# Kernel optimization log

Hardware: AMD Instinct MI355X
Metric: run time of the kernel (lower is better)

Reference implementation:

```python
import jax, jax.numpy as jnp
import numpy as np

N_NODES = 50000
N_EDGES = 800000
N_REL = 16
D = 64          # entity_dim == relation_dim == n_hidden
NEG_SLOPE = 0.01  # torch F.leaky_relu default


def setup_inputs() -> dict:
    key = jax.random.key(0)
    ks = jax.random.split(key, 12)
    s = 1.0 / np.sqrt(D)
    return {
        "node_ids": jnp.arange(N_NODES, dtype=jnp.int64) if jax.config.jax_enable_x64 else jnp.arange(N_NODES, dtype=jnp.int32),
        "relation_ids": jax.random.randint(ks[0], (N_EDGES,), 0, N_REL),
        "src": jax.random.randint(ks[1], (N_EDGES,), 0, N_NODES),
        "dst": jax.random.randint(ks[2], (N_EDGES,), 0, N_NODES),
        "entity_embed": jax.random.normal(ks[3], (N_NODES, D), jnp.float32) * s,
        "relation_embed": jax.random.normal(ks[4], (N_REL, D), jnp.float32) * s,
        "W0": jax.random.normal(ks[5], (N_REL, D, D), jnp.float32) * s,
        "W1": jax.random.normal(ks[6], (N_REL, D, D), jnp.float32) * s,
        "ra0": jax.random.normal(ks[7], (D, D), jnp.float32) * s,
        "rb0": jax.random.normal(ks[8], (D, D), jnp.float32) * s,
        "ra1": jax.random.normal(ks[9], (D, D), jnp.float32) * s,
        "rb1": jax.random.normal(ks[10], (D, D), jnp.float32) * s,
    }


def _edge_softmax(scores, dst, n_nodes):
    # segment softmax over edges grouped by destination node (DGL edge_softmax)
    m = jax.ops.segment_max(scores, dst, num_segments=n_nodes)  # [N]
    e = jnp.exp(scores - m[dst])                                # [E]
    z = jax.ops.segment_sum(e, dst, num_segments=n_nodes)       # [N]
    return e / z[dst]


def _kgat_layer(h, efeat, src, dst, etype, Wr, ra, rb, n_nodes):
    # transform every node under every relation once: [N, R, Dr]
    trans = jnp.einsum('nd,rde->nre', h, Wr)
    t_r = trans[src, etype]                   # W_r h_t  [E, Dr]
    h_r = trans[dst, etype]                   # W_r h_h  [E, Dr]
    att = jnp.sum(t_r * jnp.tanh(h_r + efeat), axis=1)  # [E]
    a = _edge_softmax(att, dst, n_nodes)                 # [E]
    # u_mul_e + sum: scatter-add weighted source features to dst
    h_nb = jax.ops.segment_sum(h[src] * a[:, None], dst, num_segments=n_nodes)
    # Bi residual
    out = (jax.nn.leaky_relu((h + h_nb) @ ra, NEG_SLOPE)
           + jax.nn.leaky_relu((h * h_nb) @ rb, NEG_SLOPE))
    return out


def reference(node_ids, relation_ids, src, dst, entity_embed, relation_embed,
              W0, W1, ra0, rb0, ra1, rb1):
    h = entity_embed[node_ids]                 # [N, D]
    efeat = relation_embed[relation_ids]       # [E, D]
    n_nodes = node_ids.shape[0]
    cache = [h]
    for Wr, ra, rb in ((W0, ra0, rb0), (W1, ra1, rb1)):
        h = _kgat_layer(h, efeat, src, dst, relation_ids, Wr, ra, rb, n_nodes)
        cache.append(h)
    return jnp.concatenate(cache, axis=1)      # [N, 3*D]
```

## Files before the change

### kernel.cpp

```cpp
#include <hip/hip_runtime.h>
#include <hip/hip_bf16.h>
#include <math.h>

#define NN 50000
#define NE 800000
#define NR 16
#define DD 64
#define OSTRIDE 192
#define QSTRIDE 1032

typedef _Float16 f16;
typedef f16 f16x8 __attribute__((ext_vector_type(8)));
typedef f16 f16x2 __attribute__((ext_vector_type(2)));
typedef __attribute__((ext_vector_type(4))) float f32x4;

__device__ inline float tanh_fast(float x) {
    return 1.f - 2.f / (__expf(2.f * x) + 1.f);
}

__device__ inline float dot2acc(f16x2 a, f16x2 b, float c) {
#if __has_builtin(__builtin_amdgcn_fdot2)
    return __builtin_amdgcn_fdot2(a, b, c, false);
#else
    return c + (float)a[0] * (float)b[0] + (float)a[1] * (float)b[1];
#endif
}

__global__ void k_deg(const int* __restrict__ dst, int* __restrict__ cnt) {
    for (int e = blockIdx.x * blockDim.x + threadIdx.x; e < NE;
         e += gridDim.x * blockDim.x)
        atomicAdd(&cnt[dst[e]], 1);
}

__global__ __launch_bounds__(256) void k_scan1(const int* __restrict__ cnt,
                                               int* __restrict__ rowptr,
                                               int* __restrict__ bsum) {
    __shared__ int sh[256];
    int b = blockIdx.x, t = threadIdx.x;
    int i = b * 256 + t;
    int v = (i < NN) ? cnt[i] : 0;
    sh[t] = v;
    __syncthreads();
    #pragma unroll
    for (int o = 1; o < 256; o <<= 1) {
        int u = (t >= o) ? sh[t - o] : 0;
        __syncthreads();
        sh[t] += u;
        __syncthreads();
    }
    if (i < NN) rowptr[i] = sh[t] - v;
    if (t == 255) bsum[b] = sh[255];
}

__global__ __launch_bounds__(256) void k_scan2(int* __restrict__ bsum, int nb) {
    __shared__ int sh[256];
    int t = threadIdx.x;
    int v = (t < nb) ? bsum[t] : 0;
    sh[t] = v;
    __syncthreads();
    #pragma unroll
    for (int o = 1; o < 256; o <<= 1) {
        int u = (t >= o) ? sh[t - o] : 0;
        __syncthreads();
        sh[t] += u;
        __syncthreads();
    }
    if (t < nb) bsum[t] = sh[t] - v;
}

__global__ __launch_bounds__(256) void k_scan3(int* __restrict__ rowptr,
                                               const int* __restrict__ bsum,
                                               int* __restrict__ cursor) {
    int b = blockIdx.x, t = threadIdx.x;
    int i = b * 256 + t;
    if (i < NN) {
        int v = rowptr[i] + bsum[b];
        rowptr[i] = v;
        cursor[i] = v;
    }
    if (i == 0) rowptr[NN] = NE;
}

__global__ void k_fill(const int* __restrict__ dst, const int* __restrict__ src,
                       const int* __restrict__ rel, int* __restrict__ cursor,
                       int* __restrict__ epack) {
    for (int e = blockIdx.x * blockDim.x + threadIdx.x; e < NE;
         e += gridDim.x * blockDim.x) {
        int pos = atomicAdd(&cursor[dst[e]], 1);
        epack[pos] = src[e] | (rel[e] << 16);
    }
}

__global__ void k_copy_h0(const int* __restrict__ node_ids,
                          const float* __restrict__ ent,
                          float* __restrict__ out,
                          f16* __restrict__ hf) {
    int i = blockIdx.x * blockDim.x + threadIdx.x;
    if (i >= NN * DD) return;
    int n = i >> 6, d = i & 63;
    float v = ent[(size_t)node_ids[n] * DD + d];
    out[(size_t)n * OSTRIDE + d] = v;
    hf[(size_t)n * DD + d] = (f16)v;
}

__global__ void k_wprep(const float* __restrict__ W, f16* __restrict__ wf,
                        f16* __restrict__ wtf) {
    int i = blockIdx.x * blockDim.x + threadIdx.x;
    if (i >= NR * DD * DD) return;
    int r = i >> 12, rem = i & 4095, d = rem >> 6, E = rem & 63;
    f16 v = (f16)W[i];
    wf[i] = v;
    wtf[(r << 12) | (E << 6) | d] = v;
}

__global__ __launch_bounds__(1024) void k_fused8(const f16* __restrict__ hf,
                                                 const f16* __restrict__ wf,
                                                 const f16* __restrict__ wtf,
                                                 const float* __restrict__ relE,
                                                 const int* __restrict__ rowptr,
                                                 const int* __restrict__ epack,
                                                 float* __restrict__ h_nb) {
    __shared__ __align__(16) f16 q_lds[16 * QSTRIDE];
    __shared__ __align__(16) f16 u_lds[16][16][72];
    int n0 = blockIdx.x * 16;
    int t  = threadIdx.x;
    int w  = t >> 6, l = t & 63;
    int l15 = l & 15, lg = l >> 4;
    int r = w;

    {
        int ar = n0 + l15; if (ar >= NN) ar = NN - 1;
        const f16* ap = hf + (size_t)ar * DD + lg * 8;
        f16x8 a0 = *(const f16x8*)ap;
        f16x8 a1 = *(const f16x8*)(ap + 32);

        f32x4 acc[4];
        #pragma unroll
        for (int nt = 0; nt < 4; ++nt) acc[nt] = (f32x4){0.f, 0.f, 0.f, 0.f};
        const f16* wtr = wtf + (r << 12);
        #pragma unroll
        for (int nt = 0; nt < 4; ++nt) {
            const f16* bp = wtr + (nt * 16 + l15) * DD + lg * 8;
            f16x8 b0 = *(const f16x8*)bp;
            f16x8 b1 = *(const f16x8*)(bp + 32);
            acc[nt] = __builtin_amdgcn_mfma_f32_16x16x32_f16(a0, b0, acc[nt], 0, 0, 0);
            acc[nt] = __builtin_amdgcn_mfma_f32_16x16x32_f16(a1, b1, acc[nt], 0, 0, 0);
        }

        #pragma unroll
        for (int nt = 0; nt < 4; ++nt) {
            int E = nt * 16 + l15;
            float er = relE[r * DD + E];
            #pragma unroll
            for (int reg = 0; reg < 4; ++reg)
                u_lds[w][lg * 4 + reg][E] = (f16)tanh_fast(acc[nt][reg] + er);
        }
        asm volatile("s_waitcnt lgkmcnt(0)" ::: "memory");

        const f16* up = &u_lds[w][l15][lg * 8];
        f16x8 u0 = *(const f16x8*)up;
        f16x8 u1 = *(const f16x8*)(up + 32);

        f32x4 q4[4];
        #pragma unroll
        for (int nt = 0; nt < 4; ++nt) q4[nt] = (f32x4){0.f, 0.f, 0.f, 0.f};
        const f16* wr = wf + (r << 12);
        #pragma unroll
        for (int nt = 0; nt < 4; ++nt) {
            const f16* bp = wr + (nt * 16 + l15) * DD + lg * 8;
            f16x8 b0 = *(const f16x8*)bp;
            f16x8 b1 = *(const f16x8*)(bp + 32);
            q4[nt] = __builtin_amdgcn_mfma_f32_16x16x32_f16(u0, b0, q4[nt], 0, 0, 0);
            q4[nt] = __builtin_amdgcn_mfma_f32_16x16x32_f16(u1, b1, q4[nt], 0, 0, 0);
        }

        #pragma unroll
        for (int reg = 0; reg < 4; ++reg) {
            f16* qp = q_lds + (lg * 4 + reg) * QSTRIDE + r * 64 + l15;
            #pragma unroll
            for (int nt = 0; nt < 4; ++nt)
                qp[nt * 16] = (f16)q4[nt][reg];
        }
    }
    __syncthreads();

    int n = n0 + w;
    if (n >= NN) return;
    const f16* ql = q_lds + w * QSTRIDE;
    int row0 = rowptr[n], row1 = rowptr[n + 1];
    int deg = row1 - row0;
    int g  = l >> 3;
    int d8 = l & 7;

    float zr = 0.f;
    float a[8] = {};

    int steps = (deg + 7) >> 3;
    for (int k = 0; k < steps; ++k) {
        int idx = row0 + (k << 3) + g;
        bool ok = idx < row1;
        int p = epack[ok ? idx : row0];
        int s = p & 0xffff, rr = p >> 16;
        f16x8 hv = *(const f16x8*)(hf + ((size_t)s << 6) + (d8 << 3));
        f16x8 qv = *(const f16x8*)(ql + (rr << 6) + (d8 << 3));
        float dp = 0.f;
        #pragma unroll
        for (int j = 0; j < 4; ++j) {
            f16x2 ha = {hv[2 * j], hv[2 * j + 1]};
            f16x2 qa = {qv[2 * j], qv[2 * j + 1]};
            dp = dot2acc(ha, qa, dp);
        }
        dp += __shfl_xor(dp, 1, 64);
        dp += __shfl_xor(dp, 2, 64);
        dp += __shfl_xor(dp, 4, 64);
        float wg = ok ? __expf(dp) : 0.f;
        zr += wg;
        #pragma unroll
        for (int j = 0; j < 8; ++j)
            a[j] = fmaf(wg, (float)hv[j], a[j]);
    }

    #pragma unroll
    for (int o = 8; o < 64; o <<= 1) {
        zr += __shfl_xor(zr, o, 64);
        #pragma unroll
        for (int j = 0; j < 8; ++j)
            a[j] += __shfl_xor(a[j], o, 64);
    }

    if (g == 0) {
        float inv = (deg > 0) ? 1.f / zr : 0.f;
        float4* dst4 = (float4*)&h_nb[((size_t)n << 6) + (d8 << 3)];
        dst4[0] = make_float4(a[0] * inv, a[1] * inv, a[2] * inv, a[3] * inv);
        dst4[1] = make_float4(a[4] * inv, a[5] * inv, a[6] * inv, a[7] * inv);
    }
}

__global__ __launch_bounds__(256) void k_out2(const float* __restrict__ h_nb,
                                              const float* __restrict__ ra,
                                              const float* __restrict__ rb,
                                              float* __restrict__ out,
                                              int off_in, int off_out,
                                              f16* __restrict__ hf) {
    __shared__ __align__(16) float v1s[64][68];
    __shared__ __align__(16) float v2s[64][68];
    __shared__ __align__(16) float ws[2][64][64];
    int t = threadIdx.x;
    int n0 = blockIdx.x * 64;

    for (int i = t; i < 1024; i += 256) {
        int ni = i >> 4, c4 = (i & 15) * 4;
        int n = n0 + ni;
        float4 hv = make_float4(0.f, 0.f, 0.f, 0.f);
        float4 nb = make_float4(0.f, 0.f, 0.f, 0.f);
        if (n < NN) {
            hv = *(const float4*)&out[(size_t)n * OSTRIDE + off_in + c4];
            nb = *(const float4*)&h_nb[(size_t)n * DD + c4];
        }
        v1s[c4 + 0][ni] = hv.x + nb.x;  v2s[c4 + 0][ni] = hv.x * nb.x;
        v1s[c4 + 1][ni] = hv.y + nb.y;  v2s[c4 + 1][ni] = hv.y * nb.y;
        v1s[c4 + 2][ni] = hv.z + nb.z;  v2s[c4 + 2][ni] = hv.z * nb.z;
        v1s[c4 + 3][ni] = hv.w + nb.w;  v2s[c4 + 3][ni] = hv.w * nb.w;
    }
    for (int i = t; i < 2048; i += 256) {
        const float* base = (i < 1024) ? ra : rb;
        int rem = i & 1023;
        float4 v = *(const float4*)&base[rem * 4];
        int k = rem >> 4, c4 = (rem & 15) * 4;
        *(float4*)&ws[i >> 10][k][c4] = v;
    }
    __syncthreads();

    int nd0 = (t >> 4) * 4;
    int c0  = (t & 15) * 4;
    float a1[4][4] = {}, a2[4][4] = {};
    #pragma unroll 8
    for (int k = 0; k < 64; ++k) {
        float4 h1 = *(const float4*)&v1s[k][nd0];
        float4 h2 = *(const float4*)&v2s[k][nd0];
        float4 wa = *(const float4*)&ws[0][k][c0];
        float4 wb = *(const float4*)&ws[1][k][c0];
        float x1[4] = {h1.x, h1.y, h1.z, h1.w};
        float x2[4] = {h2.x, h2.y, h2.z, h2.w};
        #pragma unroll
        for (int i = 0; i < 4; ++i) {
            a1[i][0] += x1[i] * wa.x; a1[i][1] += x1[i] * wa.y;
            a1[i][2] += x1[i] * wa.z; a1[i][3] += x1[i] * wa.w;
            a2[i][0] += x2[i] * wb.x; a2[i][1] += x2[i] * wb.y;
            a2[i][2] += x2[i] * wb.z; a2[i][3] += x2[i] * wb.w;
        }
    }
    #pragma unroll
    for (int i = 0; i < 4; ++i) {
        int n = n0 + nd0 + i;
        if (n >= NN) continue;
        float4 o;
        float* po = (float*)&o;
        #pragma unroll
        for (int j = 0; j < 4; ++j) {
            float u1 = a1[i][j], u2 = a2[i][j];
            u1 = u1 > 0.f ? u1 : 0.01f * u1;
            u2 = u2 > 0.f ? u2 : 0.01f * u2;
            po[j] = u1 + u2;
        }
        *(float4*)&out[(size_t)n * OSTRIDE + off_out + c0] = o;
        hf[(size_t)n * DD + c0 + 0] = (f16)o.x;
        hf[(size_t)n * DD + c0 + 1] = (f16)o.y;
        hf[(size_t)n * DD + c0 + 2] = (f16)o.z;
        hf[(size_t)n * DD + c0 + 3] = (f16)o.w;
    }
}

extern "C" void kernel_launch(void* const* d_in, const int* in_sizes, int n_in,
                              void* d_out, int out_size, void* d_ws, size_t ws_size,
                              hipStream_t stream) {
    const int*   node_ids = (const int*)d_in[0];
    const int*   rel_ids  = (const int*)d_in[1];
    const int*   src      = (const int*)d_in[2];
    const int*   dst      = (const int*)d_in[3];
    const float* ent      = (const float*)d_in[4];
    const float* relE     = (const float*)d_in[5];
    const float* W[2]  = {(const float*)d_in[6], (const float*)d_in[7]};
    const float* ra[2] = {(const float*)d_in[8], (const float*)d_in[10]};
    const float* rb[2] = {(const float*)d_in[9], (const float*)d_in[11]};
    float* out = (float*)d_out;

    const size_t hnb_bytes    = (size_t)NN * DD * sizeof(float);
    const size_t hf_bytes     = (size_t)NN * DD * sizeof(f16);
    const size_t wf_bytes     = (size_t)NR * DD * DD * sizeof(f16);
    const size_t epack_bytes  = (size_t)NE * sizeof(int);
    const size_t rowptr_bytes = (size_t)(NN + 1) * sizeof(int);
    const size_t cnt_bytes    = (size_t)NN * sizeof(int);
    const int    NB_SCAN      = (NN + 255) / 256;
    const size_t bsum_bytes   = (size_t)256 * sizeof(int);

    char* p = (char*)d_ws;
    float* h_nb   = (float*)p; p += hnb_bytes;
    f16*   hf     = (f16*)p;   p += hf_bytes;
    f16*   wf     = (f16*)p;   p += wf_bytes;
    f16*   wtf    = (f16*)p;   p += wf_bytes;
    int*   epack  = (int*)p;   p += epack_bytes;
    int*   rowptr = (int*)p;   p += rowptr_bytes;
    int*   cnt    = (int*)p;   p += cnt_bytes;
    int*   bsum   = (int*)p;   p += bsum_bytes;
    (void)ws_size;

    hipMemsetAsync(cnt, 0, cnt_bytes, stream);
    k_deg  <<<1024, 256, 0, stream>>>(dst, cnt);
    k_scan1<<<NB_SCAN, 256, 0, stream>>>(cnt, rowptr, bsum);
    k_scan2<<<1, 256, 0, stream>>>(bsum, NB_SCAN);
    k_scan3<<<NB_SCAN, 256, 0, stream>>>(rowptr, bsum, cnt);
    k_fill <<<1024, 256, 0, stream>>>(dst, src, rel_ids, cnt, epack);

    k_copy_h0<<<(NN * DD + 255) / 256, 256, 0, stream>>>(node_ids, ent, out, hf);

    for (int L = 0; L < 2; ++L) {
        int off_in = L * DD;
        int off_out = (L + 1) * DD;

        k_wprep <<<(NR * DD * DD + 255) / 256, 256, 0, stream>>>(W[L], wf, wtf);
        k_fused8<<<(NN + 15) / 16, 1024, 0, stream>>>(hf, wf, wtf, relE,
                                                      rowptr, epack, h_nb);
        k_out2  <<<(NN + 63) / 64, 256, 0, stream>>>(h_nb, ra[L], rb[L], out,
                                                     off_in, off_out, hf);
    }
}
```

Measured before the change: 412.2 us.

## Fuse bi-residual output projection into aggregation kernel using MFMA

Folds the per-node bi-residual matmuls (ra, rb) and leaky-ReLU into the fused aggregation kernel. The v1/v2 vectors go to LDS as fp16 and are multiplied with MFMA by four waves, so the fp32 h_nb round-trip through global memory and the separate fp32 FMA output kernel disappear. It adds an fp16 transpose prep kernel for ra/rb and ping-pongs two fp16 h buffers, because the fused kernel now reads the old features while writing the new ones. Risks include lower precision in the residual matmul and removed bounds checks that rely on NN being a multiple of 16.

After: 387.0 us. 1.07x faster.

```diff
diff --git a/kernel.cpp b/kernel.cpp
--- a/kernel.cpp
+++ b/kernel.cpp
@@ -11,6 +11,7 @@
 
 typedef _Float16 f16;
 typedef f16 f16x8 __attribute__((ext_vector_type(8)));
+typedef f16 f16x4 __attribute__((ext_vector_type(4)));
 typedef f16 f16x2 __attribute__((ext_vector_type(2)));
 typedef __attribute__((ext_vector_type(4))) float f32x4;
 
@@ -113,13 +114,26 @@
     wtf[(r << 12) | (E << 6) | d] = v;
 }
 
-__global__ __launch_bounds__(1024) void k_fused8(const f16* __restrict__ hf,
-                                                 const f16* __restrict__ wf,
-                                                 const f16* __restrict__ wtf,
-                                                 const float* __restrict__ relE,
-                                                 const int* __restrict__ rowptr,
-                                                 const int* __restrict__ epack,
-                                                 float* __restrict__ h_nb) {
+__global__ void k_rprep(const float* __restrict__ ra, const float* __restrict__ rb,
+                        f16* __restrict__ rat, f16* __restrict__ rbt) {
+    int i = blockIdx.x * blockDim.x + threadIdx.x;
+    if (i >= DD * DD) return;
+    int d = i >> 6, dp = i & 63;
+    rat[dp * 64 + d] = (f16)ra[i];
+    rbt[dp * 64 + d] = (f16)rb[i];
+}
+
+__global__ __launch_bounds__(1024) void k_fused10(const f16* __restrict__ hfin,
+                                                  const f16* __restrict__ wf,
+                                                  const f16* __restrict__ wtf,
+                                                  const f16* __restrict__ rat,
+                                                  const f16* __restrict__ rbt,
+                                                  const float* __restrict__ relE,
+                                                  const int* __restrict__ rowptr,
+                                                  const int* __restrict__ epack,
+                                                  float* __restrict__ out,
+                                                  int off_in, int off_out,
+                                                  f16* __restrict__ hfout) {
     __shared__ __align__(16) f16 q_lds[16 * QSTRIDE];
     __shared__ __align__(16) f16 u_lds[16][16][72];
     int n0 = blockIdx.x * 16;
@@ -129,8 +143,8 @@
     int r = w;
 
     {
-        int ar = n0 + l15; if (ar >= NN) ar = NN - 1;
-        const f16* ap = hf + (size_t)ar * DD + lg * 8;
+        int ar = n0 + l15;
+        const f16* ap = hfin + (size_t)ar * DD + lg * 8;
         f16x8 a0 = *(const f16x8*)ap;
         f16x8 a1 = *(const f16x8*)(ap + 32);
 
@@ -185,7 +199,6 @@
     __syncthreads();
 
     int n = n0 + w;
-    if (n >= NN) return;
     const f16* ql = q_lds + w * QSTRIDE;
     int row0 = rowptr[n], row1 = rowptr[n + 1];
     int deg = row1 - row0;
@@ -201,7 +214,7 @@
         bool ok = idx < row1;
         int p = epack[ok ? idx : row0];
         int s = p & 0xffff, rr = p >> 16;
-        f16x8 hv = *(const f16x8*)(hf + ((size_t)s << 6) + (d8 << 3));
+        f16x8 hv = *(const f16x8*)(hfin + ((size_t)s << 6) + (d8 << 3));
         f16x8 qv = *(const f16x8*)(ql + (rr << 6) + (d8 << 3));
         float dp = 0.f;
         #pragma unroll
@@ -230,84 +243,55 @@
 
     if (g == 0) {
         float inv = (deg > 0) ? 1.f / zr : 0.f;
-        float4* dst4 = (float4*)&h_nb[((size_t)n << 6) + (d8 << 3)];
-        dst4[0] = make_float4(a[0] * inv, a[1] * inv, a[2] * inv, a[3] * inv);
-        dst4[1] = make_float4(a[4] * inv, a[5] * inv, a[6] * inv, a[7] * inv);
-    }
-}
-
-__global__ __launch_bounds__(256) void k_out2(const float* __restrict__ h_nb,
-                                              const float* __restrict__ ra,
-                                              const float* __restrict__ rb,
-                                              float* __restrict__ out,
-                                              int off_in, int off_out,
-                                              f16* __restrict__ hf) {
-    __shared__ __align__(16) float v1s[64][68];
-    __shared__ __align__(16) float v2s[64][68];
-    __shared__ __align__(16) float ws[2][64][64];
-    int t = threadIdx.x;
-    int n0 = blockIdx.x * 64;
-
-    for (int i = t; i < 1024; i += 256) {
-        int ni = i >> 4, c4 = (i & 15) * 4;
-        int n = n0 + ni;
-        float4 hv = make_float4(0.f, 0.f, 0.f, 0.f);
-        float4 nb = make_float4(0.f, 0.f, 0.f, 0.f);
-        if (n < NN) {
-            hv = *(const float4*)&out[(size_t)n * OSTRIDE + off_in + c4];
-            nb = *(const float4*)&h_nb[(size_t)n * DD + c4];
-        }
-        v1s[c4 + 0][ni] = hv.x + nb.x;  v2s[c4 + 0][ni] = hv.x * nb.x;
-        v1s[c4 + 1][ni] = hv.y + nb.y;  v2s[c4 + 1][ni] = hv.y * nb.y;
-        v1s[c4 + 2][ni] = hv.z + nb.z;  v2s[c4 + 2][ni] = hv.z * nb.z;
-        v1s[c4 + 3][ni] = hv.w + nb.w;  v2s[c4 + 3][ni] = hv.w * nb.w;
-    }
-    for (int i = t; i < 2048; i += 256) {
-        const float* base = (i < 1024) ? ra : rb;
-        int rem = i & 1023;
-        float4 v = *(const float4*)&base[rem * 4];
-        int k = rem >> 4, c4 = (rem & 15) * 4;
-        *(float4*)&ws[i >> 10][k][c4] = v;
+        const float* hp = &out[(size_t)n * OSTRIDE + off_in + (d8 << 3)];
+        float4 h0 = *(const float4*)hp;
+        float4 h1 = *(const float4*)(hp + 4);
+        float hh[8] = {h0.x, h0.y, h0.z, h0.w, h1.x, h1.y, h1.z, h1.w};
+        f16x8 v1v, v2v;
+        #pragma unroll
+        for (int j = 0; j < 8; ++j) {
+            float nb = a[j] * inv;
+            v1v[j] = (f16)(hh[j] + nb);
+            v2v[j] = (f16)(hh[j] * nb);
+        }
+        *(f16x8*)(q_lds + w * QSTRIDE + (d8 << 3)) = v1v;
+        *(f16x8*)(q_lds + w * QSTRIDE + 256 + (d8 << 3)) = v2v;
     }
     __syncthreads();
 
-    int nd0 = (t >> 4) * 4;
-    int c0  = (t & 15) * 4;
-    float a1[4][4] = {}, a2[4][4] = {};
-    #pragma unroll 8
-    for (int k = 0; k < 64; ++k) {
-        float4 h1 = *(const float4*)&v1s[k][nd0];
-        float4 h2 = *(const float4*)&v2s[k][nd0];
-        float4 wa = *(const float4*)&ws[0][k][c0];
-        float4 wb = *(const float4*)&ws[1][k][c0];
-        float x1[4] = {h1.x, h1.y, h1.z, h1.w};
-        float x2[4] = {h2.x, h2.y, h2.z, h2.w};
-        #pragma unroll
-        for (int i = 0; i < 4; ++i) {
-            a1[i][0] += x1[i] * wa.x; a1[i][1] += x1[i] * wa.y;
-            a1[i][2] += x1[i] * wa.z; a1[i][3] += x1[i] * wa.w;
-            a2[i][0] += x2[i] * wb.x; a2[i][1] += x2[i] * wb.y;
-            a2[i][2] += x2[i] * wb.z; a2[i][3] += x2[i] * wb.w;
-        }
-    }
-    #pragma unroll
-    for (int i = 0; i < 4; ++i) {
-        int n = n0 + nd0 + i;
-        if (n >= NN) continue;
-        float4 o;
-        float* po = (float*)&o;
-        #pragma unroll
-        for (int j = 0; j < 4; ++j) {
-            float u1 = a1[i][j], u2 = a2[i][j];
+    if (w < 4) {
+        const f16* v1p = q_lds + (size_t)l15 * QSTRIDE + lg * 8;
+        f16x8 a10 = *(const f16x8*)v1p;
+        f16x8 a11 = *(const f16x8*)(v1p + 32);
+        const f16* v2p = v1p + 256;
+        f16x8 a20 = *(const f16x8*)v2p;
+        f16x8 a21 = *(const f16x8*)(v2p + 32);
+
+        const f16* bra = rat + (w * 16 + l15) * 64 + lg * 8;
+        f16x8 b10 = *(const f16x8*)bra;
+        f16x8 b11 = *(const f16x8*)(bra + 32);
+        const f16* brb = rbt + (w * 16 + l15) * 64 + lg * 8;
+        f16x8 b20 = *(const f16x8*)brb;
+        f16x8 b21 = *(const f16x8*)(brb + 32);
+
+        f32x4 o1 = (f32x4){0.f, 0.f, 0.f, 0.f};
+        f32x4 o2 = (f32x4){0.f, 0.f, 0.f, 0.f};
+        o1 = __builtin_amdgcn_mfma_f32_16x16x32_f16(a10, b10, o1, 0, 0, 0);
+        o1 = __builtin_amdgcn_mfma_f32_16x16x32_f16(a11, b11, o1, 0, 0, 0);
+        o2 = __builtin_amdgcn_mfma_f32_16x16x32_f16(a20, b20, o2, 0, 0, 0);
+        o2 = __builtin_amdgcn_mfma_f32_16x16x32_f16(a21, b21, o2, 0, 0, 0);
+
+        int dp = w * 16 + l15;
+        #pragma unroll
+        for (int reg = 0; reg < 4; ++reg) {
+            int node = n0 + lg * 4 + reg;
+            float u1 = o1[reg], u2 = o2[reg];
             u1 = u1 > 0.f ? u1 : 0.01f * u1;
             u2 = u2 > 0.f ? u2 : 0.01f * u2;
-            po[j] = u1 + u2;
-        }
-        *(float4*)&out[(size_t)n * OSTRIDE + off_out + c0] = o;
-        hf[(size_t)n * DD + c0 + 0] = (f16)o.x;
-        hf[(size_t)n * DD + c0 + 1] = (f16)o.y;
-        hf[(size_t)n * DD + c0 + 2] = (f16)o.z;
-        hf[(size_t)n * DD + c0 + 3] = (f16)o.w;
+            float v = u1 + u2;
+            out[(size_t)node * OSTRIDE + off_out + dp] = v;
+            hfout[(size_t)node * DD + dp] = (f16)v;
+        }
     }
 }
 
@@ -325,9 +309,9 @@
     const float* rb[2] = {(const float*)d_in[9], (const float*)d_in[11]};
     float* out = (float*)d_out;
 
-    const size_t hnb_bytes    = (size_t)NN * DD * sizeof(float);
     const size_t hf_bytes     = (size_t)NN * DD * sizeof(f16);
     const size_t wf_bytes     = (size_t)NR * DD * DD * sizeof(f16);
+    const size_t rt_bytes     = (size_t)DD * DD * sizeof(f16);
     const size_t epack_bytes  = (size_t)NE * sizeof(int);
     const size_t rowptr_bytes = (size_t)(NN + 1) * sizeof(int);
     const size_t cnt_bytes    = (size_t)NN * sizeof(int);
@@ -335,10 +319,12 @@
     const size_t bsum_bytes   = (size_t)256 * sizeof(int);
 
     char* p = (char*)d_ws;
-    float* h_nb   = (float*)p; p += hnb_bytes;
     f16*   hf     = (f16*)p;   p += hf_bytes;
+    f16*   hf2    = (f16*)p;   p += hf_bytes;
     f16*   wf     = (f16*)p;   p += wf_bytes;
     f16*   wtf    = (f16*)p;   p += wf_bytes;
+    f16*   rat    = (f16*)p;   p += rt_bytes;
+    f16*   rbt    = (f16*)p;   p += rt_bytes;
     int*   epack  = (int*)p;   p += epack_bytes;
     int*   rowptr = (int*)p;   p += rowptr_bytes;
     int*   cnt    = (int*)p;   p += cnt_bytes;
@@ -354,14 +340,17 @@
 
     k_copy_h0<<<(NN * DD + 255) / 256, 256, 0, stream>>>(node_ids, ent, out, hf);
 
+    f16* hin  = hf;
+    f16* hout = hf2;
     for (int L = 0; L < 2; ++L) {
         int off_in = L * DD;
         int off_out = (L + 1) * DD;
 
         k_wprep <<<(NR * DD * DD + 255) / 256, 256, 0, stream>>>(W[L], wf, wtf);
-        k_fused8<<<(NN + 15) / 16, 1024, 0, stream>>>(hf, wf, wtf, relE,
-                                                      rowptr, epack, h_nb);
-        k_out2  <<<(NN + 63) / 64, 256, 0, stream>>>(h_nb, ra[L], rb[L], out,
-                                                     off_in, off_out, hf);
-    }
-}
+        k_rprep <<<(DD * DD + 255) / 256, 256, 0, stream>>>(ra[L], rb[L], rat, rbt);
+        k_fused10<<<NN / 16, 1024, 0, stream>>>(hin, wf, wtf, rat, rbt, relE,
+                                                rowptr, epack, out,
+                                                off_in, off_out, hout);
+        f16* tmp = hin; hin = hout; hout = tmp;
+    }
+}
```
